# Kernel optimization log

Hardware: AMD Instinct MI355X
Metric: run time of the kernel (lower is better)

## Reference

```python
import jax, jax.numpy as jnp
import numpy as np

BLOCK = 32  # GGML Q8_0 block size: 32 int8 values share one scale


def setup_inputs() -> dict:
    key = jax.random.key(0)
    k1, k2, k3 = jax.random.split(key, 3)
    B, S, I, O = 2, 2048, 4096, 4096
    A = jax.random.normal(k1, (B, S, I), dtype=jnp.float32)
    # quantized weight values: stored unsigned 0..255, interpreted as signed (v - 128)
    w_q = jax.random.randint(k2, (O, I), 0, 255, dtype=jnp.int32)
    # one scale per block of 32 along infeatures
    scales = jax.random.uniform(k3, (O, I // BLOCK), dtype=jnp.float32) * 0.05
    return {"A": A, "w_q": w_q, "scales": scales}


def reference(A, w_q, scales):
    # Fused dequant + matmul (GGML Q8_0-style):
    # W[o, i] = (w_q[o, i] - 128) * scales[o, i // 32]
    O, I = w_q.shape
    q = w_q.astype(jnp.float32) - 128.0                      # [O, I]
    W = (q.reshape(O, I // BLOCK, BLOCK) * scales[:, :, None]).reshape(O, I)
    # C = A @ W^T, matching ggml mul_mat (weight is [outfeatures, infeatures])
    return jnp.einsum('bsi,oi->bso', A, W)
```

## Files before the change

kernel.cpp:

```cpp
#include <hip/hip_runtime.h>
#include <stdint.h>

typedef unsigned short u16;
typedef __bf16 bf16x8 __attribute__((ext_vector_type(8)));
typedef float f32x4 __attribute__((ext_vector_type(4)));
typedef unsigned short u16x8 __attribute__((ext_vector_type(8)));

__device__ __forceinline__ u16 f2bf(float f) {
  union { float f; uint32_t u; } x; x.f = f;
  uint32_t r = x.u + 0x7fffu + ((x.u >> 16) & 1u);
  return (u16)(r >> 16);
}

__global__ __launch_bounds__(256) void cvt_all(
    const float* __restrict__ A, u16* __restrict__ Ab, size_t n8a,
    const int* __restrict__ Wq, const float* __restrict__ S,
    u16* __restrict__ Wb, size_t n8w) {
  size_t i = (size_t)blockIdx.x * 256 + threadIdx.x;
  if (i < n8a) {
    const float4* p = (const float4*)(A + i * 8);
    float4 v0 = p[0], v1 = p[1];
    u16x8 r = { f2bf(v0.x), f2bf(v0.y), f2bf(v0.z), f2bf(v0.w),
                f2bf(v1.x), f2bf(v1.y), f2bf(v1.z), f2bf(v1.w) };
    *(u16x8*)(Ab + i * 8) = r;
  } else {
    size_t j = i - n8a;
    if (j >= n8w) return;
    const int4* p = (const int4*)(Wq + j * 8);
    int4 v0 = p[0], v1 = p[1];
    float s = S[j >> 2];
    u16x8 r = { f2bf((float)(v0.x - 128) * s), f2bf((float)(v0.y - 128) * s),
                f2bf((float)(v0.z - 128) * s), f2bf((float)(v0.w - 128) * s),
                f2bf((float)(v1.x - 128) * s), f2bf((float)(v1.y - 128) * s),
                f2bf((float)(v1.z - 128) * s), f2bf((float)(v1.w - 128) * s) };
    *(u16x8*)(Wb + j * 8) = r;
  }
}

#define BM 256
#define BN 128
#define BK 32

__device__ __forceinline__ void load_lds_16B(const void* g, void* l) {
  __builtin_amdgcn_global_load_lds(
      (const __attribute__((address_space(1))) unsigned int*)g,
      (__attribute__((address_space(3))) unsigned int*)l, 16, 0, 0);
}

template <int MODE>
__global__ __launch_bounds__(256, 2) void gemm_mode(
    const u16* __restrict__ Ab, const u16* __restrict__ Wb,
    const float* __restrict__ Af, const int* __restrict__ Wq,
    const float* __restrict__ Sc, float* __restrict__ C,
    int M, int N, int K) {
  __shared__ u16 As[BM * BK];
  __shared__ u16 Bs[BN * BK];

  const int tid = threadIdx.x;
  const int wave = tid >> 6, lane = tid & 63;
  const int m0 = blockIdx.y * BM, n0 = blockIdx.x * BN;
  const int wm = (wave & 1) * 128, wn = (wave >> 1) * 64;
  const int lrow = lane & 15, lq = lane >> 4;

  const u16* gA[4]; u16* dA[4];
  const u16* gB[2]; u16* dB[2];
  if constexpr (MODE == 0) {
    #pragma unroll
    for (int it = 0; it < 4; ++it) {
      int q = wave * 256 + it * 64 + lane;
      int row = q >> 2, s = q & 3;
      int c = (s - (row >> 1)) & 3;
      gA[it] = Ab + (size_t)(m0 + row) * K + c * 8;
      dA[it] = As + (size_t)(wave * 256 + it * 64) * 8;
    }
  }
  if constexpr (MODE <= 1) {
    #pragma unroll
    for (int it = 0; it < 2; ++it) {
      int q = wave * 128 + it * 64 + lane;
      int row = q >> 2, s = q & 3;
      int c = (s - (row >> 1)) & 3;
      gB[it] = Wb + (size_t)(n0 + row) * K + c * 8;
      dB[it] = Bs + (size_t)(wave * 128 + it * 64) * 8;
    }
  }

  const u16* fA[8]; const u16* fB[4];
  #pragma unroll
  for (int i = 0; i < 8; ++i) {
    int row = wm + i * 16 + lrow;
    int s = (lq + (row >> 1)) & 3;
    fA[i] = As + row * BK + s * 8;
  }
  #pragma unroll
  for (int j = 0; j < 4; ++j) {
    int row = wn + j * 16 + lrow;
    int s = (lq + (row >> 1)) & 3;
    fB[j] = Bs + row * BK + s * 8;
  }

  f32x4 acc[8][4] = {};

  for (int k0 = 0; k0 < K; k0 += BK) {
    if constexpr (MODE == 0) {
      #pragma unroll
      for (int it = 0; it < 4; ++it) load_lds_16B(gA[it] + k0, dA[it]);
      #pragma unroll
      for (int it = 0; it < 2; ++it) load_lds_16B(gB[it] + k0, dB[it]);
    } else {
      #pragma unroll
      for (int it = 0; it < 4; ++it) {
        int g = it * 256 + tid;
        int row = g >> 2, c8 = g & 3;
        int s = (c8 + (row >> 1)) & 3;
        const float4* p = (const float4*)(Af + (size_t)(m0 + row) * K + k0 + c8 * 8);
        float4 v0 = p[0], v1 = p[1];
        u16x8 r = { f2bf(v0.x), f2bf(v0.y), f2bf(v0.z), f2bf(v0.w),
                    f2bf(v1.x), f2bf(v1.y), f2bf(v1.z), f2bf(v1.w) };
        *(u16x8*)(As + row * BK + s * 8) = r;
      }
      if constexpr (MODE == 1) {
        #pragma unroll
        for (int it = 0; it < 2; ++it) load_lds_16B(gB[it] + k0, dB[it]);
      } else {
        #pragma unroll
        for (int it = 0; it < 2; ++it) {
          int g = it * 256 + tid;
          int row = g >> 2, c8 = g & 3;
          int s = (c8 + (row >> 1)) & 3;
          const int4* p = (const int4*)(Wq + (size_t)(n0 + row) * K + k0 + c8 * 8);
          int4 v0 = p[0], v1 = p[1];
          float sc = Sc[(size_t)(n0 + row) * (K >> 5) + (k0 >> 5)];
          u16x8 r = { f2bf((float)(v0.x - 128) * sc), f2bf((float)(v0.y - 128) * sc),
                      f2bf((float)(v0.z - 128) * sc), f2bf((float)(v0.w - 128) * sc),
                      f2bf((float)(v1.x - 128) * sc), f2bf((float)(v1.y - 128) * sc),
                      f2bf((float)(v1.z - 128) * sc), f2bf((float)(v1.w - 128) * sc) };
          *(u16x8*)(Bs + row * BK + s * 8) = r;
        }
      }
    }
    __syncthreads();

    bf16x8 a[8], b[4];
    #pragma unroll
    for (int i = 0; i < 8; ++i) a[i] = *(const bf16x8*)fA[i];
    #pragma unroll
    for (int j = 0; j < 4; ++j) b[j] = *(const bf16x8*)fB[j];
    #pragma unroll
    for (int i = 0; i < 8; ++i)
      #pragma unroll
      for (int j = 0; j < 4; ++j)
        acc[i][j] = __builtin_amdgcn_mfma_f32_16x16x32_bf16(a[i], b[j], acc[i][j], 0, 0, 0);
    __syncthreads();
  }

  #pragma unroll
  for (int i = 0; i < 8; ++i) {
    #pragma unroll
    for (int r = 0; r < 4; ++r) {
      int gm = m0 + wm + i * 16 + lq * 4 + r;
      float* crow = C + (size_t)gm * N + n0 + wn + lrow;
      #pragma unroll
      for (int j = 0; j < 4; ++j) crow[j * 16] = acc[i][j][r];
    }
  }
}

extern "C" void kernel_launch(void* const* d_in, const int* in_sizes, int n_in,
                              void* d_out, int out_size, void* d_ws, size_t ws_size,
                              hipStream_t stream) {
  const float* A  = (const float*)d_in[0];
  const int*   Wq = (const int*)d_in[1];
  const float* S  = (const float*)d_in[2];
  float* C = (float*)d_out;

  const int K = 4096;
  const int N = in_sizes[1] / K;
  const int M = in_sizes[0] / K;

  const size_t needA = (size_t)M * K * sizeof(u16);
  const size_t needW = (size_t)N * K * sizeof(u16);
  dim3 grid(N / BN, M / BM), blk(256);

  if (ws_size >= needA + needW) {
    u16* Ab = (u16*)d_ws;
    u16* Wb = (u16*)((char*)d_ws + needA);
    size_t nA8 = (size_t)M * K / 8, nW8 = (size_t)N * K / 8;
    cvt_all<<<(int)((nA8 + nW8 + 255) / 256), 256, 0, stream>>>(A, Ab, nA8, Wq, S, Wb, nW8);
    gemm_mode<0><<<grid, blk, 0, stream>>>(Ab, Wb, nullptr, nullptr, nullptr, C, M, N, K);
  } else if (ws_size >= needW) {
    u16* Wb = (u16*)d_ws;
    size_t nW8 = (size_t)N * K / 8;
    cvt_all<<<(int)((nW8 + 255) / 256), 256, 0, stream>>>(nullptr, nullptr, 0, Wq, S, Wb, nW8);
    gemm_mode<1><<<grid, blk, 0, stream>>>(nullptr, Wb, A, nullptr, nullptr, C, M, N, K);
  } else {
    gemm_mode<2><<<grid, blk, 0, stream>>>(nullptr, nullptr, A, Wq, S, C, M, N, K);
  }
}
```

Measured before the change: 302.7 us.

## Double-buffer B tiles in LDS and load A fragments directly from global memory

Adds a new GEMM kernel for the full-workspace path. B tiles are double-buffered in LDS, so the next tile's async global-to-LDS load overlaps with the MFMAs on the current one. A fragments are read straight from global memory into registers instead of being staged in LDS, and each wave now owns a 64x128 slab. This removes one barrier per step and the LDS traffic for A, but per-lane global A loads are strided across rows and may coalesce poorly or stall the MFMAs. The fallback kernels are only reorganized.

```diff
diff --git a/kernel.cpp b/kernel.cpp
--- a/kernel.cpp
+++ b/kernel.cpp
@@ -47,9 +47,102 @@
       (__attribute__((address_space(3))) unsigned int*)l, 16, 0, 0);
 }
 
+__global__ __launch_bounds__(256, 2) void gemm_dbuf(
+    const u16* __restrict__ Ab, const u16* __restrict__ Wb,
+    float* __restrict__ C, int M, int N, int K) {
+  __shared__ u16 Bs[2 * BN * BK];
+
+  const int tid = threadIdx.x;
+  const int wave = tid >> 6, lane = tid & 63;
+  const int m0 = blockIdx.y * BM, n0 = blockIdx.x * BN;
+  const int wm = wave * 64;
+  const int lrow = lane & 15, lq = lane >> 4;
+
+  const u16* pA[4];
+  #pragma unroll
+  for (int i = 0; i < 4; ++i)
+    pA[i] = Ab + (size_t)(m0 + wm + i * 16 + lrow) * K + lq * 8;
+
+  const u16* gB[2]; u16* dB[2];
+  #pragma unroll
+  for (int it = 0; it < 2; ++it) {
+    int q = wave * 128 + it * 64 + lane;
+    int row = q >> 2, s = q & 3;
+    int c = (s - (row >> 1)) & 3;
+    gB[it] = Wb + (size_t)(n0 + row) * K + c * 8;
+    dB[it] = Bs + (size_t)(wave * 128 + it * 64) * 8;
+  }
+
+  const u16* fB[8];
+  #pragma unroll
+  for (int j = 0; j < 8; ++j) {
+    int row = j * 16 + lrow;
+    int s = (lq + (row >> 1)) & 3;
+    fB[j] = Bs + row * BK + s * 8;
+  }
+
+  f32x4 acc[4][8] = {};
+  bf16x8 a0[4], a1[4];
+
+  #pragma unroll
+  for (int it = 0; it < 2; ++it) load_lds_16B(gB[it], dB[it]);
+  #pragma unroll
+  for (int i = 0; i < 4; ++i) a0[i] = *(const bf16x8*)(pA[i]);
+  __syncthreads();
+
+  const int NT = K / BK;
+  for (int t = 0; t < NT; t += 2) {
+    {
+      const int kn = (t + 1) * BK;
+      #pragma unroll
+      for (int it = 0; it < 2; ++it) load_lds_16B(gB[it] + kn, dB[it] + BN * BK);
+      #pragma unroll
+      for (int i = 0; i < 4; ++i) a1[i] = *(const bf16x8*)(pA[i] + kn);
+      bf16x8 b[8];
+      #pragma unroll
+      for (int j = 0; j < 8; ++j) b[j] = *(const bf16x8*)fB[j];
+      #pragma unroll
+      for (int i = 0; i < 4; ++i)
+        #pragma unroll
+        for (int j = 0; j < 8; ++j)
+          acc[i][j] = __builtin_amdgcn_mfma_f32_16x16x32_bf16(a0[i], b[j], acc[i][j], 0, 0, 0);
+      __syncthreads();
+    }
+    {
+      const int kn = (t + 2) * BK;
+      if (t + 2 < NT) {
+        #pragma unroll
+        for (int it = 0; it < 2; ++it) load_lds_16B(gB[it] + kn, dB[it]);
+        #pragma unroll
+        for (int i = 0; i < 4; ++i) a0[i] = *(const bf16x8*)(pA[i] + kn);
+      }
+      bf16x8 b[8];
+      #pragma unroll
+      for (int j = 0; j < 8; ++j) b[j] = *(const bf16x8*)(fB[j] + BN * BK);
+      #pragma unroll
+      for (int i = 0; i < 4; ++i)
+        #pragma unroll
+        for (int j = 0; j < 8; ++j)
+          acc[i][j] = __builtin_amdgcn_mfma_f32_16x16x32_bf16(a1[i], b[j], acc[i][j], 0, 0, 0);
+      __syncthreads();
+    }
+  }
+
+  #pragma unroll
+  for (int i = 0; i < 4; ++i) {
+    #pragma unroll
+    for (int r = 0; r < 4; ++r) {
+      int gm = m0 + wm + i * 16 + lq * 4 + r;
+      float* crow = C + (size_t)gm * N + n0 + lrow;
+      #pragma unroll
+      for (int j = 0; j < 8; ++j) crow[j * 16] = acc[i][j][r];
+    }
+  }
+}
+
 template <int MODE>
-__global__ __launch_bounds__(256, 2) void gemm_mode(
-    const u16* __restrict__ Ab, const u16* __restrict__ Wb,
+__global__ __launch_bounds__(256, 2) void gemm_fb(
+    const u16* __restrict__ Wb,
     const float* __restrict__ Af, const int* __restrict__ Wq,
     const float* __restrict__ Sc, float* __restrict__ C,
     int M, int N, int K) {
@@ -62,19 +155,8 @@
   const int wm = (wave & 1) * 128, wn = (wave >> 1) * 64;
   const int lrow = lane & 15, lq = lane >> 4;
 
-  const u16* gA[4]; u16* dA[4];
   const u16* gB[2]; u16* dB[2];
-  if constexpr (MODE == 0) {
-    #pragma unroll
-    for (int it = 0; it < 4; ++it) {
-      int q = wave * 256 + it * 64 + lane;
-      int row = q >> 2, s = q & 3;
-      int c = (s - (row >> 1)) & 3;
-      gA[it] = Ab + (size_t)(m0 + row) * K + c * 8;
-      dA[it] = As + (size_t)(wave * 256 + it * 64) * 8;
-    }
-  }
-  if constexpr (MODE <= 1) {
+  if constexpr (MODE == 1) {
     #pragma unroll
     for (int it = 0; it < 2; ++it) {
       int q = wave * 128 + it * 64 + lane;
@@ -102,41 +184,34 @@
   f32x4 acc[8][4] = {};
 
   for (int k0 = 0; k0 < K; k0 += BK) {
-    if constexpr (MODE == 0) {
-      #pragma unroll
-      for (int it = 0; it < 4; ++it) load_lds_16B(gA[it] + k0, dA[it]);
+    #pragma unroll
+    for (int it = 0; it < 4; ++it) {
+      int g = it * 256 + tid;
+      int row = g >> 2, c8 = g & 3;
+      int s = (c8 + (row >> 1)) & 3;
+      const float4* p = (const float4*)(Af + (size_t)(m0 + row) * K + k0 + c8 * 8);
+      float4 v0 = p[0], v1 = p[1];
+      u16x8 r = { f2bf(v0.x), f2bf(v0.y), f2bf(v0.z), f2bf(v0.w),
+                  f2bf(v1.x), f2bf(v1.y), f2bf(v1.z), f2bf(v1.w) };
+      *(u16x8*)(As + row * BK + s * 8) = r;
+    }
+    if constexpr (MODE == 1) {
       #pragma unroll
       for (int it = 0; it < 2; ++it) load_lds_16B(gB[it] + k0, dB[it]);
     } else {
       #pragma unroll
-      for (int it = 0; it < 4; ++it) {
+      for (int it = 0; it < 2; ++it) {
         int g = it * 256 + tid;
         int row = g >> 2, c8 = g & 3;
         int s = (c8 + (row >> 1)) & 3;
-        const float4* p = (const float4*)(Af + (size_t)(m0 + row) * K + k0 + c8 * 8);
-        float4 v0 = p[0], v1 = p[1];
-        u16x8 r = { f2bf(v0.x), f2bf(v0.y), f2bf(v0.z), f2bf(v0.w),
-                    f2bf(v1.x), f2bf(v1.y), f2bf(v1.z), f2bf(v1.w) };
-        *(u16x8*)(As + row * BK + s * 8) = r;
-      }
-      if constexpr (MODE == 1) {
-        #pragma unroll
-        for (int it = 0; it < 2; ++it) load_lds_16B(gB[it] + k0, dB[it]);
-      } else {
-        #pragma unroll
-        for (int it = 0; it < 2; ++it) {
-          int g = it * 256 + tid;
-          int row = g >> 2, c8 = g & 3;
-          int s = (c8 + (row >> 1)) & 3;
-          const int4* p = (const int4*)(Wq + (size_t)(n0 + row) * K + k0 + c8 * 8);
-          int4 v0 = p[0], v1 = p[1];
-          float sc = Sc[(size_t)(n0 + row) * (K >> 5) + (k0 >> 5)];
-          u16x8 r = { f2bf((float)(v0.x - 128) * sc), f2bf((float)(v0.y - 128) * sc),
-                      f2bf((float)(v0.z - 128) * sc), f2bf((float)(v0.w - 128) * sc),
-                      f2bf((float)(v1.x - 128) * sc), f2bf((float)(v1.y - 128) * sc),
-                      f2bf((float)(v1.z - 128) * sc), f2bf((float)(v1.w - 128) * sc) };
-          *(u16x8*)(Bs + row * BK + s * 8) = r;
-        }
+        const int4* p = (const int4*)(Wq + (size_t)(n0 + row) * K + k0 + c8 * 8);
+        int4 v0 = p[0], v1 = p[1];
+        float sc = Sc[(size_t)(n0 + row) * (K >> 5) + (k0 >> 5)];
+        u16x8 r = { f2bf((float)(v0.x - 128) * sc), f2bf((float)(v0.y - 128) * sc),
+                    f2bf((float)(v0.z - 128) * sc), f2bf((float)(v0.w - 128) * sc),
+                    f2bf((float)(v1.x - 128) * sc), f2bf((float)(v1.y - 128) * sc),
+                    f2bf((float)(v1.z - 128) * sc), f2bf((float)(v1.w - 128) * sc) };
+        *(u16x8*)(Bs + row * BK + s * 8) = r;
       }
     }
     __syncthreads();
@@ -187,13 +262,13 @@
     u16* Wb = (u16*)((char*)d_ws + needA);
     size_t nA8 = (size_t)M * K / 8, nW8 = (size_t)N * K / 8;
     cvt_all<<<(int)((nA8 + nW8 + 255) / 256), 256, 0, stream>>>(A, Ab, nA8, Wq, S, Wb, nW8);
-    gemm_mode<0><<<grid, blk, 0, stream>>>(Ab, Wb, nullptr, nullptr, nullptr, C, M, N, K);
+    gemm_dbuf<<<grid, blk, 0, stream>>>(Ab, Wb, C, M, N, K);
   } else if (ws_size >= needW) {
     u16* Wb = (u16*)d_ws;
     size_t nW8 = (size_t)N * K / 8;
     cvt_all<<<(int)((nW8 + 255) / 256), 256, 0, stream>>>(nullptr, nullptr, 0, Wq, S, Wb, nW8);
-    gemm_mode<1><<<grid, blk, 0, stream>>>(nullptr, Wb, A, nullptr, nullptr, C, M, N, K);
+    gemm_fb<1><<<grid, blk, 0, stream>>>(Wb, A, nullptr, nullptr, C, M, N, K);
   } else {
-    gemm_mode<2><<<grid, blk, 0, stream>>>(nullptr, nullptr, A, Wq, S, C, M, N, K);
-  }
-}
+    gemm_fb<2><<<grid, blk, 0, stream>>>(nullptr, A, Wq, S, C, M, N, K);
+  }
+}
```

Measured after the change: 348.9 us. +15.3%, slower.
